# Optimization experiments

Hardware: AMD Instinct MI355X
Metric: run time of the kernel (lower is better)

Reference implementation:

```python
import jax, jax.numpy as jnp
import numpy as np
from jax import lax

B, H_IMG, W_IMG = 512, 812, 40
HID = 128
NUM_CLASSES = 12
LSTM_IN = 32 * ((W_IMG - 5) // 2 + 1)  # 32 channels * 18 = 576


def setup_inputs() -> dict:
    key = jax.random.key(0)
    ks = jax.random.split(key, 20)
    s = 0.05
    inp = {
        "x": jax.random.normal(ks[0], (B, 1, H_IMG, W_IMG), jnp.float32),
        "conv_w": jax.random.normal(ks[1], (32, 1, 20, 5), jnp.float32) * s,
        "conv_b": jax.random.normal(ks[2], (32,), jnp.float32) * s,
        "Wih0": jax.random.normal(ks[3], (4 * HID, LSTM_IN), jnp.float32) * s,
        "Whh0": jax.random.normal(ks[4], (4 * HID, HID), jnp.float32) * s,
        "bih0": jax.random.normal(ks[5], (4 * HID,), jnp.float32) * s,
        "bhh0": jax.random.normal(ks[6], (4 * HID,), jnp.float32) * s,
        "Wih1": jax.random.normal(ks[7], (4 * HID, HID), jnp.float32) * s,
        "Whh1": jax.random.normal(ks[8], (4 * HID, HID), jnp.float32) * s,
        "bih1": jax.random.normal(ks[9], (4 * HID,), jnp.float32) * s,
        "bhh1": jax.random.normal(ks[10], (4 * HID,), jnp.float32) * s,
        "W_att": jax.random.normal(ks[11], (HID, HID), jnp.float32) * s,
        "b_att": jax.random.normal(ks[12], (HID,), jnp.float32) * s,
        "v_att": jax.random.normal(ks[13], (HID,), jnp.float32) * s,
        "W1": jax.random.normal(ks[14], (64, HID), jnp.float32) * s,
        "b1": jax.random.normal(ks[15], (64,), jnp.float32) * s,
        "W2": jax.random.normal(ks[16], (NUM_CLASSES, 64), jnp.float32) * s,
        "b2": jax.random.normal(ks[17], (NUM_CLASSES,), jnp.float32) * s,
    }
    return inp


def _lstm_layer(seq, Wih, Whh, bih, bhh):
    # seq: (T, B, I); PyTorch gate order i, f, g, o
    T, Bn, _ = seq.shape
    Hd = Whh.shape[1]
    x_proj = jnp.einsum('tbi,gi->tbg', seq, Wih) + bih + bhh  # (T,B,4H)

    def step(carry, xg):
        h, c = carry
        g = xg + h @ Whh.T
        i, f, gg, o = jnp.split(g, 4, axis=-1)
        c = jax.nn.sigmoid(f) * c + jax.nn.sigmoid(i) * jnp.tanh(gg)
        h = jax.nn.sigmoid(o) * jnp.tanh(c)
        return (h, c), h

    init = (jnp.zeros((Bn, Hd), seq.dtype), jnp.zeros((Bn, Hd), seq.dtype))
    _, hs = lax.scan(step, init, x_proj)
    return hs  # (T,B,H)


def _forward(x, conv_w, conv_b, Wih0, Whh0, bih0, bhh0, Wih1, Whh1, bih1, bhh1,
             W_att, b_att, v_att, W1, b1, W2, b2):
    # Conv2d(1->32, k=(20,5), s=(8,2)) + ReLU
    y = lax.conv_general_dilated(x, conv_w, (8, 2), 'VALID',
                                 dimension_numbers=('NCHW', 'OIHW', 'NCHW'))
    y = jax.nn.relu(y + conv_b[None, :, None, None])  # (B,32,T,W')
    b, c, t, w = y.shape
    # permute(0,2,3,1).view(b,t,-1).permute(1,0,2) -> (T,B,W'*32)
    seq = jnp.transpose(y, (2, 0, 3, 1)).reshape(t, b, w * c)
    # 2-layer LSTM (inter-layer dropout=0.2 inactive at eval)
    h1 = _lstm_layer(seq, Wih0, Whh0, bih0, bhh0)
    h2 = _lstm_layer(h1, Wih1, Whh1, bih1, bhh1)
    # additive attention pooling over time
    squish = jnp.tanh(jnp.einsum('tbh,hk->tbk', h2, W_att) + b_att)  # (T,B,H)
    attn = jnp.einsum('tbh,h->tb', squish, v_att)                     # (T,B)
    w_att_n = jax.nn.softmax(attn, axis=0)                            # softmax over T
    pooled = jnp.einsum('tb,tbh->bh', w_att_n, h2)                    # (B,H)
    # dnn1 -> (dropout inactive at eval) -> output
    hdn = pooled @ W1.T + b1
    return hdn @ W2.T + b2  # (B,num_classes)


def reference(x, conv_w, conv_b, Wih0, Whh0, bih0, bhh0, Wih1, Whh1, bih1, bhh1,
              W_att, b_att, v_att, W1, b1, W2, b2):
    return _forward(x, conv_w, conv_b, Wih0, Whh0, bih0, bhh0, Wih1, Whh1,
                    bih1, bhh1, W_att, b_att, v_att, W1, b1, W2, b2)
```

## Files before the change

kernel.cpp:

```cpp
#include <hip/hip_runtime.h>
#include <stdint.h>


#define T_STEPS 100
#define BATCH   512
#define HIDD    128
#define GATES   512
#define LSTMIN  576
#define HIMG    812
#define WIMG    40

typedef __attribute__((ext_vector_type(8))) short bf16x8;
typedef __attribute__((ext_vector_type(4))) float f32x4;
typedef __attribute__((ext_vector_type(2))) __fp16 f16x2;
typedef unsigned long long ull;

__device__ inline unsigned short f2bf(float f) {
  unsigned u = __float_as_uint(f);
  unsigned r = (u + 0x7fffu + ((u >> 16) & 1u)) >> 16;
  return (unsigned short)r;
}
__device__ inline unsigned pk_bf16(float a, float b) {
#if __has_builtin(__builtin_amdgcn_cvt_pk_bf16_f32)
  auto r = __builtin_amdgcn_cvt_pk_bf16_f32(a, b);
  return __builtin_bit_cast(unsigned, r);
#else
  return (unsigned)f2bf(a) | ((unsigned)f2bf(b) << 16);
#endif
}
__device__ inline float bf2f(unsigned short b) {
  return __uint_as_float(((unsigned)b) << 16);
}
__device__ inline float fsigm(float x) {
  float e = __expf(-x);
  return __builtin_amdgcn_rcpf(1.f + e);
}
__device__ inline float ftanh(float x) {
  float e = __expf(2.f * x);
  return (e - 1.f) * __builtin_amdgcn_rcpf(e + 1.f);
}
__device__ inline void lds_barrier() {
  asm volatile("s_waitcnt lgkmcnt(0)" ::: "memory");
  __builtin_amdgcn_s_barrier();
}
__device__ inline void wait_flag(int* fp, int need) {
  if ((threadIdx.x & 63) == 0) {
    while (__hip_atomic_load(fp, __ATOMIC_RELAXED, __HIP_MEMORY_SCOPE_AGENT) < need)
      __builtin_amdgcn_s_sleep(2);
  }
  asm volatile("" ::: "memory");
}

__global__ void prep_kernel(const float* __restrict__ Wih0, const float* __restrict__ Whh0,
                            const float* __restrict__ Wih1, const float* __restrict__ Whh1,
                            const float* __restrict__ Watt, const float* __restrict__ convw,
                            const float* __restrict__ bih0, const float* __restrict__ bhh0,
                            const float* __restrict__ bih1, const float* __restrict__ bhh1,
                            unsigned short* __restrict__ wih0b, unsigned short* __restrict__ whh0b,
                            unsigned short* __restrict__ wih1b, unsigned short* __restrict__ whh1b,
                            unsigned short* __restrict__ wattb, f16x2* __restrict__ wpair,
                            float* __restrict__ bias0, float* __restrict__ bias1,
                            int* __restrict__ flags) {
  int tid = blockIdx.x * blockDim.x + threadIdx.x;
  int stride = gridDim.x * blockDim.x;
  for (int i = tid; i < GATES * LSTMIN; i += stride) wih0b[i] = f2bf(Wih0[i]);
  for (int i = tid; i < GATES * HIDD; i += stride) whh0b[i] = f2bf(Whh0[i]);
  for (int i = tid; i < GATES * HIDD; i += stride) wih1b[i] = f2bf(Wih1[i]);
  for (int i = tid; i < GATES * HIDD; i += stride) whh1b[i] = f2bf(Whh1[i]);
  for (int i = tid; i < HIDD * HIDD; i += stride) {
    int j = i >> 7, k = i & 127;
    wattb[i] = f2bf(Watt[k * HIDD + j]);
  }
  for (int i = tid; i < 50 * 32; i += stride) {
    int k2 = i >> 5, c = i & 31;
    int kh2 = k2 / 5, kw = k2 % 5;
    float lo = convw[c * 100 + (2 * kh2) * 5 + kw];
    float hi = convw[c * 100 + (2 * kh2 + 1) * 5 + kw];
    wpair[i] = __builtin_amdgcn_cvt_pkrtz(lo, hi);
  }
  for (int i = tid; i < GATES; i += stride) bias0[i] = bih0[i] + bhh0[i];
  for (int i = tid; i < GATES; i += stride) bias1[i] = bih1[i] + bhh1[i];
  for (int i = tid; i < 32; i += stride) flags[i] = 0;
}

__global__ __launch_bounds__(256) void conv_kernel(const float* __restrict__ x,
                                                   const f16x2* __restrict__ wpair,
                                                   const float* __restrict__ convb,
                                                   unsigned short* __restrict__ seq) {
  __shared__ f16x2 imgp[106 * WIMG];
  const int b = blockIdx.x;
  const int chunk = blockIdx.y;
  const int t0 = chunk * 25;
  const float* src = x + (size_t)b * (HIMG * WIMG) + (size_t)(8 * t0) * WIMG;
  for (int i = threadIdx.x; i < 106 * WIMG; i += 256) {
    int r2 = i / WIMG, c = i % WIMG;
    float lo = src[(2 * r2) * WIMG + c];
    float hi = src[(2 * r2 + 1) * WIMG + c];
    imgp[i] = __builtin_amdgcn_cvt_pkrtz(lo, hi);
  }
  __syncthreads();
  for (int p = threadIdx.x; p < 450; p += 256) {
    int tl = p / 18, wp = p % 18;
    int t = t0 + tl;
    float acc[32];
#pragma unroll
    for (int c = 0; c < 32; ++c) acc[c] = 0.f;
    const f16x2* ibase = imgp + (4 * tl) * WIMG + 2 * wp;
#pragma unroll 2
    for (int kh2 = 0; kh2 < 10; ++kh2) {
#pragma unroll
      for (int kw = 0; kw < 5; ++kw) {
        f16x2 iv = ibase[kh2 * WIMG + kw];
        const f16x2* wk = wpair + (kh2 * 5 + kw) * 32;
#pragma unroll
        for (int c = 0; c < 32; ++c)
          acc[c] = __builtin_amdgcn_fdot2(iv, wk[c], acc[c], false);
      }
    }
    unsigned short* o = seq + ((size_t)(t * BATCH + b)) * LSTMIN + wp * 32;
#pragma unroll
    for (int c = 0; c < 32; ++c) {
      float v = acc[c] + convb[c];
      o[c] = f2bf(v > 0.f ? v : 0.f);
    }
  }
}

template <int KDIM>
__global__ __launch_bounds__(256) void gemm_xp_kernel(const unsigned short* __restrict__ A,
                                                      const unsigned short* __restrict__ Bw,
                                                      const float* __restrict__ bias,
                                                      unsigned short* __restrict__ Xp) {
  __shared__ __align__(16) unsigned short As[128 * 32];
  __shared__ __align__(16) unsigned short Bs[128 * 32];
  const int tid = threadIdx.x;
  const int lane = tid & 63;
  const int w = tid >> 6;
  const int col16 = lane & 15;
  const int q = lane >> 4;
  const int n0 = blockIdx.x * 128;
  const int m0 = blockIdx.y * 128;
  const int wm = (w & 1) * 64;
  const int wn = (w >> 1) * 64;
  f32x4 acc[4][4] = {};
  const int r = tid >> 2;
  const int sw = ((tid & 3) ^ (r & 3)) * 8;
  const unsigned wslot = (unsigned)w * 512;
  const unsigned short* ga = A + (size_t)(m0 + r) * KDIM + sw;
  const unsigned short* gb = Bw + (size_t)(n0 + r) * KDIM + sw;
  for (int k0 = 0; k0 < KDIM; k0 += 32) {
    __syncthreads();
    __builtin_amdgcn_global_load_lds((const __attribute__((address_space(1))) void*)(ga + k0),
                                     (__attribute__((address_space(3))) void*)(As + wslot), 16, 0, 0);
    __builtin_amdgcn_global_load_lds((const __attribute__((address_space(1))) void*)(ga + k0 + (size_t)64 * KDIM),
                                     (__attribute__((address_space(3))) void*)(As + wslot + 2048), 16, 0, 0);
    __builtin_amdgcn_global_load_lds((const __attribute__((address_space(1))) void*)(gb + k0),
                                     (__attribute__((address_space(3))) void*)(Bs + wslot), 16, 0, 0);
    __builtin_amdgcn_global_load_lds((const __attribute__((address_space(1))) void*)(gb + k0 + (size_t)64 * KDIM),
                                     (__attribute__((address_space(3))) void*)(Bs + wslot + 2048), 16, 0, 0);
    __syncthreads();
    bf16x8 af[4], bv[4];
#pragma unroll
    for (int i = 0; i < 4; ++i) {
      int ra = wm + i * 16 + col16;
      af[i] = *(const bf16x8*)(As + ra * 32 + ((q ^ (ra & 3)) * 8));
      int rb2 = wn + i * 16 + col16;
      bv[i] = *(const bf16x8*)(Bs + rb2 * 32 + ((q ^ (rb2 & 3)) * 8));
    }
#pragma unroll
    for (int i = 0; i < 4; ++i)
#pragma unroll
      for (int j = 0; j < 4; ++j)
        acc[i][j] = __builtin_amdgcn_mfma_f32_16x16x32_bf16(af[i], bv[j], acc[i][j], 0, 0, 0);
  }
#pragma unroll
  for (int ct = 0; ct < 4; ++ct) {
    int n = n0 + wn + ct * 16 + col16;
    float bvv = bias[n];
    int wS = (n >> 4) & 7;
    int ntS = n >> 7;
    int c16S = n & 15;
#pragma unroll
    for (int rt = 0; rt < 4; ++rt) {
      int m = m0 + wm + rt * 16 + q * 4;
      int t = m >> 9;
      int bb = m & 511;
      int blk = bb >> 4;
      int r16 = bb & 15;
      ushort4 u;
      u.x = f2bf(acc[rt][ct][0] + bvv);
      u.y = f2bf(acc[rt][ct][1] + bvv);
      u.z = f2bf(acc[rt][ct][2] + bvv);
      u.w = f2bf(acc[rt][ct][3] + bvv);
      size_t tile = (((size_t)t * 32 + blk) * 8 + wS) * 4 + ntS;
      *(ushort4*)(Xp + tile * 256 + c16S * 16 + r16) = u;
    }
  }
}

__global__ __launch_bounds__(512, 1) void scan_pipe_kernel(
    const unsigned short* __restrict__ Xp0, const unsigned short* __restrict__ Whh0,
    const unsigned short* __restrict__ Wih1, const float* __restrict__ bias1,
    unsigned short* __restrict__ Xp1, const unsigned short* __restrict__ Whh1,
    unsigned short* __restrict__ hout, int* __restrict__ flags) {
  __shared__ __align__(16) unsigned short hb[2][16 * 136];
  const int tid = threadIdx.x;
  const int lane = tid & 63;
  const int w = tid >> 6;
  const int col16 = lane & 15;
  const int q = lane >> 4;
  const bool producer = blockIdx.x < 32;
  const int blk = producer ? (int)blockIdx.x : (int)blockIdx.x - 32;
  const int rb = blk * 16;
  const int hc = w * 16 + col16;
  const int srow = tid >> 5;
  const int scol = (tid & 31) * 4;
  int* flagp = flags + blk;

  if (producer) {
    bf16x8 bfrag[4][4], bfrag2[4][4];
    const unsigned short* xpb[4];
    ull* xob[4];
    float biasn[4];
#pragma unroll
    for (int nt = 0; nt < 4; ++nt) {
      int cn = nt * HIDD + hc;
#pragma unroll
      for (int ks = 0; ks < 4; ++ks) {
        bfrag[nt][ks] = *(const bf16x8*)(Whh0 + (size_t)cn * HIDD + ks * 32 + q * 8);
        bfrag2[nt][ks] = *(const bf16x8*)(Wih1 + (size_t)cn * HIDD + ks * 32 + q * 8);
      }
      biasn[nt] = bias1[cn];
      size_t tile = (((size_t)blk) * 8 + w) * 4 + nt;
      xpb[nt] = Xp0 + tile * 256 + col16 * 16 + q * 4;
      xob[nt] = (ull*)(Xp1 + tile * 256 + col16 * 16 + q * 4);
    }
    uint2 xb[2][4];
#pragma unroll
    for (int nt = 0; nt < 4; ++nt) xb[0][nt] = *(const uint2*)(xpb[nt]);
#pragma unroll
    for (int nt = 0; nt < 4; ++nt) xb[1][nt] = *(const uint2*)(xpb[nt] + GATES * BATCH);
    for (int i = tid; i < 2 * 16 * 136; i += 512) hb[0][i] = 0;
    float cst[4] = {0.f, 0.f, 0.f, 0.f};
    ull pend[4] = {0, 0, 0, 0};
    lds_barrier();

#pragma unroll 4
    for (int t = 0; t < T_STEPS; ++t) {
      if (t >= 2) {
#pragma unroll
        for (int nt = 0; nt < 4; ++nt)
          __hip_atomic_store(xob[nt] + (size_t)(t - 2) * (GATES * BATCH / 4), pend[nt],
                             __ATOMIC_RELAXED, __HIP_MEMORY_SCOPE_AGENT);
      }
      asm volatile("" ::: "memory");
      const int s = t & 1;
      uint2 xv[4];
#pragma unroll
      for (int nt = 0; nt < 4; ++nt) xv[nt] = xb[s][nt];
      if (t + 2 < T_STEPS) {
#pragma unroll
        for (int nt = 0; nt < 4; ++nt)
          xb[s][nt] = *(const uint2*)(xpb[nt] + (size_t)(t + 2) * (GATES * BATCH));
      }
      asm volatile("" ::: "memory");
      const int pb = (t & 1) ^ 1;
      bf16x8 af[4];
#pragma unroll
      for (int ks = 0; ks < 4; ++ks)
        af[ks] = *(const bf16x8*)(hb[pb] + col16 * 136 + ks * 32 + q * 8);
      f32x4 acc[4];
#pragma unroll
      for (int nt = 0; nt < 4; ++nt) {
        acc[nt][0] = __uint_as_float(xv[nt].x << 16);
        acc[nt][1] = __uint_as_float(xv[nt].x & 0xffff0000u);
        acc[nt][2] = __uint_as_float(xv[nt].y << 16);
        acc[nt][3] = __uint_as_float(xv[nt].y & 0xffff0000u);
      }
#pragma unroll
      for (int ks = 0; ks < 4; ++ks)
#pragma unroll
        for (int nt = 0; nt < 4; ++nt)
          acc[nt] = __builtin_amdgcn_mfma_f32_16x16x32_bf16(af[ks], bfrag[nt][ks], acc[nt], 0, 0, 0);
      f32x4 acc2[4];
#pragma unroll
      for (int nt = 0; nt < 4; ++nt) acc2[nt] = f32x4{0.f, 0.f, 0.f, 0.f};
#pragma unroll
      for (int ks = 0; ks < 4; ++ks)
#pragma unroll
        for (int nt = 0; nt < 4; ++nt)
          acc2[nt] = __builtin_amdgcn_mfma_f32_16x16x32_bf16(af[ks], bfrag2[nt][ks], acc2[nt], 0, 0, 0);
      unsigned short hv[4];
#pragma unroll
      for (int rr = 0; rr < 4; ++rr) {
        float pi = acc[0][rr], pf = acc[1][rr];
        float pg = acc[2][rr], po = acc[3][rr];
        float cc = fsigm(pf) * cst[rr] + fsigm(pi) * ftanh(pg);
        cst[rr] = cc;
        hv[rr] = f2bf(fsigm(po) * ftanh(cc));
      }
#pragma unroll
      for (int nt = 0; nt < 4; ++nt) {
        unsigned lo = pk_bf16(acc2[nt][0] + biasn[nt], acc2[nt][1] + biasn[nt]);
        unsigned hi = pk_bf16(acc2[nt][2] + biasn[nt], acc2[nt][3] + biasn[nt]);
        pend[nt] = (ull)lo | ((ull)hi << 32);
      }
#pragma unroll
      for (int rr = 0; rr < 4; ++rr)
        hb[t & 1][(q * 4 + rr) * 136 + hc] = hv[rr];
      if ((t & 3) == 3 && t < 99) {
        asm volatile("s_waitcnt vmcnt(4) lgkmcnt(0)\ns_barrier" ::: "memory");
        if (tid == 0)
          __hip_atomic_store(flagp, t, __ATOMIC_RELAXED, __HIP_MEMORY_SCOPE_AGENT);
      } else {
        lds_barrier();
      }
    }
#pragma unroll
    for (int nt = 0; nt < 4; ++nt)
      __hip_atomic_store(xob[nt] + (size_t)98 * (GATES * BATCH / 4), pend[nt],
                         __ATOMIC_RELAXED, __HIP_MEMORY_SCOPE_AGENT);
    bf16x8 af[4];
#pragma unroll
    for (int ks = 0; ks < 4; ++ks)
      af[ks] = *(const bf16x8*)(hb[(T_STEPS - 1) & 1] + col16 * 136 + ks * 32 + q * 8);
    f32x4 acc2[4];
#pragma unroll
    for (int nt = 0; nt < 4; ++nt) acc2[nt] = f32x4{0.f, 0.f, 0.f, 0.f};
#pragma unroll
    for (int ks = 0; ks < 4; ++ks)
#pragma unroll
      for (int nt = 0; nt < 4; ++nt)
        acc2[nt] = __builtin_amdgcn_mfma_f32_16x16x32_bf16(af[ks], bfrag2[nt][ks], acc2[nt], 0, 0, 0);
#pragma unroll
    for (int nt = 0; nt < 4; ++nt) {
      unsigned lo = pk_bf16(acc2[nt][0] + biasn[nt], acc2[nt][1] + biasn[nt]);
      unsigned hi = pk_bf16(acc2[nt][2] + biasn[nt], acc2[nt][3] + biasn[nt]);
      __hip_atomic_store(xob[nt] + (size_t)99 * (GATES * BATCH / 4),
                         (ull)lo | ((ull)hi << 32),
                         __ATOMIC_RELAXED, __HIP_MEMORY_SCOPE_AGENT);
    }
    asm volatile("s_waitcnt vmcnt(0) lgkmcnt(0)\ns_barrier" ::: "memory");
    if (tid == 0)
      __hip_atomic_store(flagp, 101, __ATOMIC_RELAXED, __HIP_MEMORY_SCOPE_AGENT);
  } else {
    bf16x8 bfrag[4][4];
    ull* xpb[4];
#pragma unroll
    for (int nt = 0; nt < 4; ++nt) {
      int cn = nt * HIDD + hc;
#pragma unroll
      for (int ks = 0; ks < 4; ++ks)
        bfrag[nt][ks] = *(const bf16x8*)(Whh1 + (size_t)cn * HIDD + ks * 32 + q * 8);
      size_t tile = (((size_t)blk) * 8 + w) * 4 + nt;
      xpb[nt] = (ull*)(Xp1 + tile * 256 + col16 * 16 + q * 4);
    }
    for (int i = tid; i < 2 * 16 * 136; i += 512) hb[0][i] = 0;
    wait_flag(flagp, 7);
    ull xb[2][4];
#pragma unroll
    for (int nt = 0; nt < 4; ++nt)
      xb[0][nt] = __hip_atomic_load(xpb[nt], __ATOMIC_RELAXED, __HIP_MEMORY_SCOPE_AGENT);
#pragma unroll
    for (int nt = 0; nt < 4; ++nt)
      xb[1][nt] = __hip_atomic_load(xpb[nt] + (GATES * BATCH / 4), __ATOMIC_RELAXED, __HIP_MEMORY_SCOPE_AGENT);
    float cst[4] = {0.f, 0.f, 0.f, 0.f};
    lds_barrier();

#pragma unroll 4
    for (int t = 0; t < T_STEPS; ++t) {
      if (t > 0 && (t & 3) == 0) {
        int need = t + 7;
        if (need > 101) need = 101;
        wait_flag(flagp, need);
      }
      const int pb = (t & 1) ^ 1;
      bf16x8 af[4];
#pragma unroll
      for (int ks = 0; ks < 4; ++ks)
        af[ks] = *(const bf16x8*)(hb[pb] + col16 * 136 + ks * 32 + q * 8);
      if (t > 0) {
        ushort4 hx = *(const ushort4*)(hb[pb] + srow * 136 + scol);
        *(ushort4*)(hout + ((size_t)((t - 1) * BATCH) + rb + srow) * HIDD + scol) = hx;
      }
      const int s = t & 1;
      ull xv[4];
#pragma unroll
      for (int nt = 0; nt < 4; ++nt) xv[nt] = xb[s][nt];
      if (t + 2 < T_STEPS) {
#pragma unroll
        for (int nt = 0; nt < 4; ++nt)
          xb[s][nt] = __hip_atomic_load(xpb[nt] + (size_t)(t + 2) * (GATES * BATCH / 4),
                                        __ATOMIC_RELAXED, __HIP_MEMORY_SCOPE_AGENT);
      }
      f32x4 acc[4];
#pragma unroll
      for (int nt = 0; nt < 4; ++nt) {
        unsigned lo = (unsigned)xv[nt];
        unsigned hi = (unsigned)(xv[nt] >> 32);
        acc[nt][0] = __uint_as_float(lo << 16);
        acc[nt][1] = __uint_as_float(lo & 0xffff0000u);
        acc[nt][2] = __uint_as_float(hi << 16);
        acc[nt][3] = __uint_as_float(hi & 0xffff0000u);
      }
#pragma unroll
      for (int ks = 0; ks < 4; ++ks)
#pragma unroll
        for (int nt = 0; nt < 4; ++nt)
          acc[nt] = __builtin_amdgcn_mfma_f32_16x16x32_bf16(af[ks], bfrag[nt][ks], acc[nt], 0, 0, 0);
      unsigned short hv[4];
#pragma unroll
      for (int rr = 0; rr < 4; ++rr) {
        float pi = acc[0][rr], pf = acc[1][rr];
        float pg = acc[2][rr], po = acc[3][rr];
        float cc = fsigm(pf) * cst[rr] + fsigm(pi) * ftanh(pg);
        cst[rr] = cc;
        hv[rr] = f2bf(fsigm(po) * ftanh(cc));
      }
#pragma unroll
      for (int rr = 0; rr < 4; ++rr)
        hb[t & 1][(q * 4 + rr) * 136 + hc] = hv[rr];
      lds_barrier();
    }
    ushort4 hx = *(const ushort4*)(hb[(T_STEPS - 1) & 1] + srow * 136 + scol);
    *(ushort4*)(hout + ((size_t)((T_STEPS - 1) * BATCH) + rb + srow) * HIDD + scol) = hx;
  }
}

__global__ __launch_bounds__(256) void gemm_att_kernel(const unsigned short* __restrict__ A,
                                                       const unsigned short* __restrict__ Bw,
                                                       const float* __restrict__ b_att,
                                                       const float* __restrict__ v_att,
                                                       float* __restrict__ scores) {
  __shared__ __align__(16) unsigned short As[128 * 32];
  __shared__ __align__(16) unsigned short Bs[128 * 32];
  __shared__ float s_red[128];
  const int tid = threadIdx.x;
  const int lane = tid & 63;
  const int w = tid >> 6;
  const int col16 = lane & 15;
  const int q = lane >> 4;
  const int m0 = blockIdx.y * 128;
  const int wm = (w & 1) * 64;
  const int wn = (w >> 1) * 64;
  f32x4 acc[4][4] = {};
  const int r = tid >> 2;
  const int sw = ((tid & 3) ^ (r & 3)) * 8;
  const unsigned wslot = (unsigned)w * 512;
  const unsigned short* ga = A + (size_t)(m0 + r) * HIDD + sw;
  const unsigned short* gb = Bw + (size_t)r * HIDD + sw;
  for (int k0 = 0; k0 < HIDD; k0 += 32) {
    __syncthreads();
    __builtin_amdgcn_global_load_lds((const __attribute__((address_space(1))) void*)(ga + k0),
                                     (__attribute__((address_space(3))) void*)(As + wslot), 16, 0, 0);
    __builtin_amdgcn_global_load_lds((const __attribute__((address_space(1))) void*)(ga + k0 + (size_t)64 * HIDD),
                                     (__attribute__((address_space(3))) void*)(As + wslot + 2048), 16, 0, 0);
    __builtin_amdgcn_global_load_lds((const __attribute__((address_space(1))) void*)(gb + k0),
                                     (__attribute__((address_space(3))) void*)(Bs + wslot), 16, 0, 0);
    __builtin_amdgcn_global_load_lds((const __attribute__((address_space(1))) void*)(gb + k0 + (size_t)64 * HIDD),
                                     (__attribute__((address_space(3))) void*)(Bs + wslot + 2048), 16, 0, 0);
    __syncthreads();
    bf16x8 af[4], bv[4];
#pragma unroll
    for (int i = 0; i < 4; ++i) {
      int ra = wm + i * 16 + col16;
      af[i] = *(const bf16x8*)(As + ra * 32 + ((q ^ (ra & 3)) * 8));
      int rb2 = wn + i * 16 + col16;
      bv[i] = *(const bf16x8*)(Bs + rb2 * 32 + ((q ^ (rb2 & 3)) * 8));
    }
#pragma unroll
    for (int i = 0; i < 4; ++i)
#pragma unroll
      for (int j = 0; j < 4; ++j)
        acc[i][j] = __builtin_amdgcn_mfma_f32_16x16x32_bf16(af[i], bv[j], acc[i][j], 0, 0, 0);
  }
  if (tid < 128) s_red[tid] = 0.f;
  float rs[4][4];
#pragma unroll
  for (int rt = 0; rt < 4; ++rt)
#pragma unroll
    for (int rr = 0; rr < 4; ++rr) rs[rt][rr] = 0.f;
#pragma unroll
  for (int ct = 0; ct < 4; ++ct) {
    int n = wn + ct * 16 + col16;
    float bvv = b_att[n], vv = v_att[n];
#pragma unroll
    for (int rt = 0; rt < 4; ++rt)
#pragma unroll
      for (int rr = 0; rr < 4; ++rr) {
        float xv2 = acc[rt][ct][rr] + bvv;
        float e = __expf(2.f * xv2);
        rs[rt][rr] += vv * (e - 1.f) * __builtin_amdgcn_rcpf(e + 1.f);
      }
  }
#pragma unroll
  for (int off = 1; off < 16; off <<= 1)
#pragma unroll
    for (int rt = 0; rt < 4; ++rt)
#pragma unroll
      for (int rr = 0; rr < 4; ++rr) rs[rt][rr] += __shfl_xor(rs[rt][rr], off, 64);
  __syncthreads();
  if (col16 == 0) {
#pragma unroll
    for (int rt = 0; rt < 4; ++rt)
#pragma unroll
      for (int rr = 0; rr < 4; ++rr)
        atomicAdd(&s_red[wm + rt * 16 + q * 4 + rr], rs[rt][rr]);
  }
  __syncthreads();
  if (tid < 128) scores[m0 + tid] = s_red[tid];
}

__global__ __launch_bounds__(128) void final_kernel(const float* __restrict__ scores,
                                                    const unsigned short* __restrict__ h2,
                                                    const float* __restrict__ W1, const float* __restrict__ b1,
                                                    const float* __restrict__ W2, const float* __restrict__ b2,
                                                    float* __restrict__ out) {
  const int b = blockIdx.x;
  const int tid = threadIdx.x;
  __shared__ float wj[T_STEPS];
  __shared__ float red[128];
  __shared__ float pooled[128];
  __shared__ float hdn[64];
  float sv = (tid < T_STEPS) ? scores[tid * BATCH + b] : -1e30f;
  red[tid] = sv;
  __syncthreads();
#pragma unroll
  for (int off = 64; off > 0; off >>= 1) {
    if (tid < off) red[tid] = fmaxf(red[tid], red[tid + off]);
    __syncthreads();
  }
  float mx = red[0];
  __syncthreads();
  float ev = (tid < T_STEPS) ? __expf(sv - mx) : 0.f;
  red[tid] = ev;
  __syncthreads();
#pragma unroll
  for (int off = 64; off > 0; off >>= 1) {
    if (tid < off) red[tid] += red[tid + off];
    __syncthreads();
  }
  float inv = 1.0f / red[0];
  if (tid < T_STEPS) wj[tid] = ev * inv;
  __syncthreads();
  float p = 0.f;
  for (int t = 0; t < T_STEPS; ++t)
    p += wj[t] * bf2f(h2[((size_t)(t * BATCH + b)) * HIDD + tid]);
  pooled[tid] = p;
  __syncthreads();
  if (tid < 64) {
    float a = b1[tid];
    for (int h = 0; h < 128; ++h) a = fmaf(W1[tid * 128 + h], pooled[h], a);
    hdn[tid] = a;
  }
  __syncthreads();
  if (tid < 12) {
    float a = b2[tid];
    for (int j = 0; j < 64; ++j) a = fmaf(W2[tid * 64 + j], hdn[j], a);
    out[b * 12 + tid] = a;
  }
}

extern "C" void kernel_launch(void* const* d_in, const int* in_sizes, int n_in,
                              void* d_out, int out_size, void* d_ws, size_t ws_size,
                              hipStream_t stream) {
  (void)in_sizes; (void)n_in; (void)out_size; (void)ws_size;
  const float* x      = (const float*)d_in[0];
  const float* conv_w = (const float*)d_in[1];
  const float* conv_b = (const float*)d_in[2];
  const float* Wih0   = (const float*)d_in[3];
  const float* Whh0   = (const float*)d_in[4];
  const float* bih0   = (const float*)d_in[5];
  const float* bhh0   = (const float*)d_in[6];
  const float* Wih1   = (const float*)d_in[7];
  const float* Whh1   = (const float*)d_in[8];
  const float* bih1   = (const float*)d_in[9];
  const float* bhh1   = (const float*)d_in[10];
  const float* W_att  = (const float*)d_in[11];
  const float* b_att  = (const float*)d_in[12];
  const float* v_att  = (const float*)d_in[13];
  const float* W1     = (const float*)d_in[14];
  const float* b1     = (const float*)d_in[15];
  const float* W2     = (const float*)d_in[16];
  const float* b2     = (const float*)d_in[17];

  char* ws = (char*)d_ws;
  size_t off = 0;
  auto carve = [&](size_t bytes) { char* p = ws + off; off += (bytes + 255) & ~(size_t)255; return p; };
  unsigned short* seq    = (unsigned short*)carve((size_t)T_STEPS * BATCH * LSTMIN * 2);
  unsigned short* xp0    = (unsigned short*)carve((size_t)T_STEPS * GATES * BATCH * 2);
  unsigned short* h2     = (unsigned short*)carve((size_t)T_STEPS * BATCH * HIDD * 2);
  float*          scores = (float*)carve((size_t)T_STEPS * BATCH * 4);
  unsigned short* wih0b  = (unsigned short*)carve((size_t)GATES * LSTMIN * 2);
  unsigned short* whh0b  = (unsigned short*)carve((size_t)GATES * HIDD * 2);
  unsigned short* wih1b  = (unsigned short*)carve((size_t)GATES * HIDD * 2);
  unsigned short* whh1b  = (unsigned short*)carve((size_t)GATES * HIDD * 2);
  unsigned short* wattb  = (unsigned short*)carve((size_t)HIDD * HIDD * 2);
  f16x2*          wpair  = (f16x2*)carve(50 * 32 * 4);
  float*          bias0  = (float*)carve(GATES * 4);
  float*          bias1  = (float*)carve(GATES * 4);
  int*            flags  = (int*)carve(32 * 4);
  unsigned short* xp1 = seq;

  prep_kernel<<<256, 256, 0, stream>>>(Wih0, Whh0, Wih1, Whh1, W_att, conv_w,
                                       bih0, bhh0, bih1, bhh1,
                                       wih0b, whh0b, wih1b, whh1b, wattb, wpair,
                                       bias0, bias1, flags);
  conv_kernel<<<dim3(512, 4), 256, 0, stream>>>(x, wpair, conv_b, seq);
  gemm_xp_kernel<LSTMIN><<<dim3(4, 400), 256, 0, stream>>>(seq, wih0b, bias0, xp0);
  scan_pipe_kernel<<<64, 512, 0, stream>>>(xp0, whh0b, wih1b, bias1, xp1, whh1b, h2, flags);
  gemm_att_kernel<<<dim3(1, 400), 256, 0, stream>>>(h2, wattb, b_att, v_att, scores);
  final_kernel<<<512, 128, 0, stream>>>(scores, h2, W1, b1, W2, b2, (float*)d_out);
}
```

Before: 412.6 us.

## Split scan block warps into recurrence and side-task roles with 32-column ownership

The pipelined LSTM scan kernel now gives warps two roles. In the layer-0 block, four warps run the Whh0 recurrence, each owning 32 hidden columns across all four gates, while the other four warps compute the Wih1 projection one step behind and publish it. In the layer-1 block, four warps run the recurrence and four only copy h out to global memory. The Xp tile layout in the input GEMM is reordered to match the new per-warp ownership, launch bounds allow two blocks per CU, and the flag thresholds change. This takes the projection and store work off the recurrence critical path, at the cost of doubling per-warp MFMA and register load on the recurrence warps.

```diff
diff --git a/kernel.cpp b/kernel.cpp
--- a/kernel.cpp
+++ b/kernel.cpp
@@ -177,28 +177,30 @@
   for (int ct = 0; ct < 4; ++ct) {
     int n = n0 + wn + ct * 16 + col16;
     float bvv = bias[n];
-    int wS = (n >> 4) & 7;
-    int ntS = n >> 7;
+    int g = n >> 7;
+    int rr2 = n & 127;
+    int wqS = rr2 >> 5;
+    int ntS = g * 2 + ((rr2 >> 4) & 1);
     int c16S = n & 15;
 #pragma unroll
     for (int rt = 0; rt < 4; ++rt) {
       int m = m0 + wm + rt * 16 + q * 4;
       int t = m >> 9;
       int bb = m & 511;
-      int blk = bb >> 4;
+      int blkS = bb >> 4;
       int r16 = bb & 15;
       ushort4 u;
       u.x = f2bf(acc[rt][ct][0] + bvv);
       u.y = f2bf(acc[rt][ct][1] + bvv);
       u.z = f2bf(acc[rt][ct][2] + bvv);
       u.w = f2bf(acc[rt][ct][3] + bvv);
-      size_t tile = (((size_t)t * 32 + blk) * 8 + wS) * 4 + ntS;
+      size_t tile = (((size_t)t * 32 + blkS) * 4 + wqS) * 8 + ntS;
       *(ushort4*)(Xp + tile * 256 + c16S * 16 + r16) = u;
     }
   }
 }
 
-__global__ __launch_bounds__(512, 1) void scan_pipe_kernel(
+__global__ __launch_bounds__(512, 2) void scan_pipe_kernel(
     const unsigned short* __restrict__ Xp0, const unsigned short* __restrict__ Whh0,
     const unsigned short* __restrict__ Wih1, const float* __restrict__ bias1,
     unsigned short* __restrict__ Xp1, const unsigned short* __restrict__ Whh1,
@@ -207,223 +209,250 @@
   const int tid = threadIdx.x;
   const int lane = tid & 63;
   const int w = tid >> 6;
+  const int wq = w & 3;
+  const int role = w >> 2;
   const int col16 = lane & 15;
   const int q = lane >> 4;
   const bool producer = blockIdx.x < 32;
   const int blk = producer ? (int)blockIdx.x : (int)blockIdx.x - 32;
   const int rb = blk * 16;
-  const int hc = w * 16 + col16;
-  const int srow = tid >> 5;
-  const int scol = (tid & 31) * 4;
   int* flagp = flags + blk;
+  const size_t TSTRIDE = (size_t)GATES * BATCH;
+  const size_t TSTRIDE8 = TSTRIDE / 4;
+
+  {
+    unsigned short* hz = (unsigned short*)hb;
+    for (int i = tid; i < 2 * 16 * 136; i += 512) hz[i] = 0;
+  }
 
   if (producer) {
-    bf16x8 bfrag[4][4], bfrag2[4][4];
-    const unsigned short* xpb[4];
-    ull* xob[4];
-    float biasn[4];
-#pragma unroll
-    for (int nt = 0; nt < 4; ++nt) {
-      int cn = nt * HIDD + hc;
-#pragma unroll
-      for (int ks = 0; ks < 4; ++ks) {
-        bfrag[nt][ks] = *(const bf16x8*)(Whh0 + (size_t)cn * HIDD + ks * 32 + q * 8);
-        bfrag2[nt][ks] = *(const bf16x8*)(Wih1 + (size_t)cn * HIDD + ks * 32 + q * 8);
-      }
-      biasn[nt] = bias1[cn];
-      size_t tile = (((size_t)blk) * 8 + w) * 4 + nt;
-      xpb[nt] = Xp0 + tile * 256 + col16 * 16 + q * 4;
-      xob[nt] = (ull*)(Xp1 + tile * 256 + col16 * 16 + q * 4);
+    if (role == 0) {
+      bf16x8 bfrag[8][4];
+      const unsigned short* xpb[8];
+#pragma unroll
+      for (int nt = 0; nt < 8; ++nt) {
+        int cn = (nt >> 1) * HIDD + wq * 32 + (nt & 1) * 16 + col16;
+#pragma unroll
+        for (int ks = 0; ks < 4; ++ks)
+          bfrag[nt][ks] = *(const bf16x8*)(Whh0 + (size_t)cn * HIDD + ks * 32 + q * 8);
+        size_t tile = (((size_t)blk) * 4 + wq) * 8 + nt;
+        xpb[nt] = Xp0 + tile * 256 + col16 * 16 + q * 4;
+      }
+      uint2 xb[2][8];
+#pragma unroll
+      for (int nt = 0; nt < 8; ++nt) xb[0][nt] = *(const uint2*)(xpb[nt]);
+#pragma unroll
+      for (int nt = 0; nt < 8; ++nt) xb[1][nt] = *(const uint2*)(xpb[nt] + TSTRIDE);
+      float cst[8] = {0.f, 0.f, 0.f, 0.f, 0.f, 0.f, 0.f, 0.f};
+      lds_barrier();
+#pragma unroll 2
+      for (int t = 0; t < T_STEPS; ++t) {
+        const int s = t & 1;
+        uint2 xv[8];
+#pragma unroll
+        for (int nt = 0; nt < 8; ++nt) xv[nt] = xb[s][nt];
+        if (t + 2 < T_STEPS) {
+#pragma unroll
+          for (int nt = 0; nt < 8; ++nt)
+            xb[s][nt] = *(const uint2*)(xpb[nt] + (size_t)(t + 2) * TSTRIDE);
+        }
+        bf16x8 af[4];
+#pragma unroll
+        for (int ks = 0; ks < 4; ++ks)
+          af[ks] = *(const bf16x8*)(hb[s ^ 1] + col16 * 136 + ks * 32 + q * 8);
+        f32x4 acc[8];
+#pragma unroll
+        for (int nt = 0; nt < 8; ++nt) {
+          acc[nt][0] = __uint_as_float(xv[nt].x << 16);
+          acc[nt][1] = __uint_as_float(xv[nt].x & 0xffff0000u);
+          acc[nt][2] = __uint_as_float(xv[nt].y << 16);
+          acc[nt][3] = __uint_as_float(xv[nt].y & 0xffff0000u);
+        }
+#pragma unroll
+        for (int ks = 0; ks < 4; ++ks)
+#pragma unroll
+          for (int nt = 0; nt < 8; ++nt)
+            acc[nt] = __builtin_amdgcn_mfma_f32_16x16x32_bf16(af[ks], bfrag[nt][ks], acc[nt], 0, 0, 0);
+#pragma unroll
+        for (int hh = 0; hh < 2; ++hh)
+#pragma unroll
+          for (int rr = 0; rr < 4; ++rr) {
+            int idx = hh * 4 + rr;
+            float pi = acc[0 + hh][rr];
+            float pf = acc[2 + hh][rr];
+            float pg = acc[4 + hh][rr];
+            float po = acc[6 + hh][rr];
+            float cc = fsigm(pf) * cst[idx] + fsigm(pi) * ftanh(pg);
+            cst[idx] = cc;
+            hb[s][(q * 4 + rr) * 136 + wq * 32 + hh * 16 + col16] = f2bf(fsigm(po) * ftanh(cc));
+          }
+        lds_barrier();
+      }
+      lds_barrier();
+    } else {
+      bf16x8 bfrag2[8][4];
+      float biasn[8];
+      ull* xob[8];
+#pragma unroll
+      for (int nt = 0; nt < 8; ++nt) {
+        int cn = (nt >> 1) * HIDD + wq * 32 + (nt & 1) * 16 + col16;
+#pragma unroll
+        for (int ks = 0; ks < 4; ++ks)
+          bfrag2[nt][ks] = *(const bf16x8*)(Wih1 + (size_t)cn * HIDD + ks * 32 + q * 8);
+        biasn[nt] = bias1[cn];
+        size_t tile = (((size_t)blk) * 4 + wq) * 8 + nt;
+        xob[nt] = (ull*)(Xp1 + tile * 256 + col16 * 16 + q * 4);
+      }
+      lds_barrier();
+#pragma unroll 2
+      for (int t = 0; t < T_STEPS; ++t) {
+        const int s = t & 1;
+        if (t > 0) {
+          bf16x8 af[4];
+#pragma unroll
+          for (int ks = 0; ks < 4; ++ks)
+            af[ks] = *(const bf16x8*)(hb[s ^ 1] + col16 * 136 + ks * 32 + q * 8);
+          f32x4 acc2[8];
+#pragma unroll
+          for (int nt = 0; nt < 8; ++nt) acc2[nt] = f32x4{0.f, 0.f, 0.f, 0.f};
+#pragma unroll
+          for (int ks = 0; ks < 4; ++ks)
+#pragma unroll
+            for (int nt = 0; nt < 8; ++nt)
+              acc2[nt] = __builtin_amdgcn_mfma_f32_16x16x32_bf16(af[ks], bfrag2[nt][ks], acc2[nt], 0, 0, 0);
+#pragma unroll
+          for (int nt = 0; nt < 8; ++nt) {
+            unsigned lo = pk_bf16(acc2[nt][0] + biasn[nt], acc2[nt][1] + biasn[nt]);
+            unsigned hi = pk_bf16(acc2[nt][2] + biasn[nt], acc2[nt][3] + biasn[nt]);
+            __hip_atomic_store(xob[nt] + (size_t)(t - 1) * TSTRIDE8,
+                               (ull)lo | ((ull)hi << 32),
+                               __ATOMIC_RELAXED, __HIP_MEMORY_SCOPE_AGENT);
+          }
+        }
+        if ((t & 3) == 3) {
+          asm volatile("s_waitcnt vmcnt(0) lgkmcnt(0)\ns_barrier" ::: "memory");
+          if (tid == 256)
+            __hip_atomic_store(flagp, t, __ATOMIC_RELAXED, __HIP_MEMORY_SCOPE_AGENT);
+        } else {
+          lds_barrier();
+        }
+      }
+      {
+        bf16x8 af[4];
+#pragma unroll
+        for (int ks = 0; ks < 4; ++ks)
+          af[ks] = *(const bf16x8*)(hb[(T_STEPS - 1) & 1] + col16 * 136 + ks * 32 + q * 8);
+        f32x4 acc2[8];
+#pragma unroll
+        for (int nt = 0; nt < 8; ++nt) acc2[nt] = f32x4{0.f, 0.f, 0.f, 0.f};
+#pragma unroll
+        for (int ks = 0; ks < 4; ++ks)
+#pragma unroll
+          for (int nt = 0; nt < 8; ++nt)
+            acc2[nt] = __builtin_amdgcn_mfma_f32_16x16x32_bf16(af[ks], bfrag2[nt][ks], acc2[nt], 0, 0, 0);
+#pragma unroll
+        for (int nt = 0; nt < 8; ++nt) {
+          unsigned lo = pk_bf16(acc2[nt][0] + biasn[nt], acc2[nt][1] + biasn[nt]);
+          unsigned hi = pk_bf16(acc2[nt][2] + biasn[nt], acc2[nt][3] + biasn[nt]);
+          __hip_atomic_store(xob[nt] + (size_t)(T_STEPS - 1) * TSTRIDE8,
+                             (ull)lo | ((ull)hi << 32),
+                             __ATOMIC_RELAXED, __HIP_MEMORY_SCOPE_AGENT);
+        }
+        asm volatile("s_waitcnt vmcnt(0) lgkmcnt(0)\ns_barrier" ::: "memory");
+        if (tid == 256)
+          __hip_atomic_store(flagp, 100, __ATOMIC_RELAXED, __HIP_MEMORY_SCOPE_AGENT);
+      }
     }
-    uint2 xb[2][4];
-#pragma unroll
-    for (int nt = 0; nt < 4; ++nt) xb[0][nt] = *(const uint2*)(xpb[nt]);
-#pragma unroll
-    for (int nt = 0; nt < 4; ++nt) xb[1][nt] = *(const uint2*)(xpb[nt] + GATES * BATCH);
-    for (int i = tid; i < 2 * 16 * 136; i += 512) hb[0][i] = 0;
-    float cst[4] = {0.f, 0.f, 0.f, 0.f};
-    ull pend[4] = {0, 0, 0, 0};
-    lds_barrier();
-
-#pragma unroll 4
-    for (int t = 0; t < T_STEPS; ++t) {
-      if (t >= 2) {
-#pragma unroll
-        for (int nt = 0; nt < 4; ++nt)
-          __hip_atomic_store(xob[nt] + (size_t)(t - 2) * (GATES * BATCH / 4), pend[nt],
-                             __ATOMIC_RELAXED, __HIP_MEMORY_SCOPE_AGENT);
-      }
-      asm volatile("" ::: "memory");
-      const int s = t & 1;
-      uint2 xv[4];
-#pragma unroll
-      for (int nt = 0; nt < 4; ++nt) xv[nt] = xb[s][nt];
-      if (t + 2 < T_STEPS) {
-#pragma unroll
-        for (int nt = 0; nt < 4; ++nt)
-          xb[s][nt] = *(const uint2*)(xpb[nt] + (size_t)(t + 2) * (GATES * BATCH));
-      }
-      asm volatile("" ::: "memory");
-      const int pb = (t & 1) ^ 1;
-      bf16x8 af[4];
-#pragma unroll
-      for (int ks = 0; ks < 4; ++ks)
-        af[ks] = *(const bf16x8*)(hb[pb] + col16 * 136 + ks * 32 + q * 8);
-      f32x4 acc[4];
-#pragma unroll
-      for (int nt = 0; nt < 4; ++nt) {
-        acc[nt][0] = __uint_as_float(xv[nt].x << 16);
-        acc[nt][1] = __uint_as_float(xv[nt].x & 0xffff0000u);
-        acc[nt][2] = __uint_as_float(xv[nt].y << 16);
-        acc[nt][3] = __uint_as_float(xv[nt].y & 0xffff0000u);
-      }
-#pragma unroll
-      for (int ks = 0; ks < 4; ++ks)
-#pragma unroll
-        for (int nt = 0; nt < 4; ++nt)
-          acc[nt] = __builtin_amdgcn_mfma_f32_16x16x32_bf16(af[ks], bfrag[nt][ks], acc[nt], 0, 0, 0);
-      f32x4 acc2[4];
-#pragma unroll
-      for (int nt = 0; nt < 4; ++nt) acc2[nt] = f32x4{0.f, 0.f, 0.f, 0.f};
-#pragma unroll
-      for (int ks = 0; ks < 4; ++ks)
-#pragma unroll
-        for (int nt = 0; nt < 4; ++nt)
-          acc2[nt] = __builtin_amdgcn_mfma_f32_16x16x32_bf16(af[ks], bfrag2[nt][ks], acc2[nt], 0, 0, 0);
-      unsigned short hv[4];
-#pragma unroll
-      for (int rr = 0; rr < 4; ++rr) {
-        float pi = acc[0][rr], pf = acc[1][rr];
-        float pg = acc[2][rr], po = acc[3][rr];
-        float cc = fsigm(pf) * cst[rr] + fsigm(pi) * ftanh(pg);
-        cst[rr] = cc;
-        hv[rr] = f2bf(fsigm(po) * ftanh(cc));
-      }
-#pragma unroll
-      for (int nt = 0; nt < 4; ++nt) {
-        unsigned lo = pk_bf16(acc2[nt][0] + biasn[nt], acc2[nt][1] + biasn[nt]);
-        unsigned hi = pk_bf16(acc2[nt][2] + biasn[nt], acc2[nt][3] + biasn[nt]);
-        pend[nt] = (ull)lo | ((ull)hi << 32);
-      }
-#pragma unroll
-      for (int rr = 0; rr < 4; ++rr)
-        hb[t & 1][(q * 4 + rr) * 136 + hc] = hv[rr];
-      if ((t & 3) == 3 && t < 99) {
-        asm volatile("s_waitcnt vmcnt(4) lgkmcnt(0)\ns_barrier" ::: "memory");
-        if (tid == 0)
-          __hip_atomic_store(flagp, t, __ATOMIC_RELAXED, __HIP_MEMORY_SCOPE_AGENT);
-      } else {
+  } else {
+    if (role == 0) {
+      bf16x8 bfrag[8][4];
+      ull* xpb[8];
+#pragma unroll
+      for (int nt = 0; nt < 8; ++nt) {
+        int cn = (nt >> 1) * HIDD + wq * 32 + (nt & 1) * 16 + col16;
+#pragma unroll
+        for (int ks = 0; ks < 4; ++ks)
+          bfrag[nt][ks] = *(const bf16x8*)(Whh1 + (size_t)cn * HIDD + ks * 32 + q * 8);
+        size_t tile = (((size_t)blk) * 4 + wq) * 8 + nt;
+        xpb[nt] = (ull*)(Xp1 + tile * 256 + col16 * 16 + q * 4);
+      }
+      wait_flag(flagp, 6);
+      ull xb[2][8];
+#pragma unroll
+      for (int nt = 0; nt < 8; ++nt)
+        xb[0][nt] = __hip_atomic_load(xpb[nt], __ATOMIC_RELAXED, __HIP_MEMORY_SCOPE_AGENT);
+#pragma unroll
+      for (int nt = 0; nt < 8; ++nt)
+        xb[1][nt] = __hip_atomic_load(xpb[nt] + TSTRIDE8, __ATOMIC_RELAXED, __HIP_MEMORY_SCOPE_AGENT);
+      float cst[8] = {0.f, 0.f, 0.f, 0.f, 0.f, 0.f, 0.f, 0.f};
+      lds_barrier();
+#pragma unroll 2
+      for (int t = 0; t < T_STEPS; ++t) {
+        if (t > 0 && (t & 3) == 0) {
+          int need = t + 6;
+          if (need > 100) need = 100;
+          wait_flag(flagp, need);
+        }
+        const int s = t & 1;
+        ull xv[8];
+#pragma unroll
+        for (int nt = 0; nt < 8; ++nt) xv[nt] = xb[s][nt];
+        if (t + 2 < T_STEPS) {
+#pragma unroll
+          for (int nt = 0; nt < 8; ++nt)
+            xb[s][nt] = __hip_atomic_load(xpb[nt] + (size_t)(t + 2) * TSTRIDE8,
+                                          __ATOMIC_RELAXED, __HIP_MEMORY_SCOPE_AGENT);
+        }
+        bf16x8 af[4];
+#pragma unroll
+        for (int ks = 0; ks < 4; ++ks)
+          af[ks] = *(const bf16x8*)(hb[s ^ 1] + col16 * 136 + ks * 32 + q * 8);
+        f32x4 acc[8];
+#pragma unroll
+        for (int nt = 0; nt < 8; ++nt) {
+          unsigned lo = (unsigned)xv[nt];
+          unsigned hi = (unsigned)(xv[nt] >> 32);
+          acc[nt][0] = __uint_as_float(lo << 16);
+          acc[nt][1] = __uint_as_float(lo & 0xffff0000u);
+          acc[nt][2] = __uint_as_float(hi << 16);
+          acc[nt][3] = __uint_as_float(hi & 0xffff0000u);
+        }
+#pragma unroll
+        for (int ks = 0; ks < 4; ++ks)
+#pragma unroll
+          for (int nt = 0; nt < 8; ++nt)
+            acc[nt] = __builtin_amdgcn_mfma_f32_16x16x32_bf16(af[ks], bfrag[nt][ks], acc[nt], 0, 0, 0);
+#pragma unroll
+        for (int hh = 0; hh < 2; ++hh)
+#pragma unroll
+          for (int rr = 0; rr < 4; ++rr) {
+            int idx = hh * 4 + rr;
+            float pi = acc[0 + hh][rr];
+            float pf = acc[2 + hh][rr];
+            float pg = acc[4 + hh][rr];
+            float po = acc[6 + hh][rr];
+            float cc = fsigm(pf) * cst[idx] + fsigm(pi) * ftanh(pg);
+            cst[idx] = cc;
+            hb[s][(q * 4 + rr) * 136 + wq * 32 + hh * 16 + col16] = f2bf(fsigm(po) * ftanh(cc));
+          }
         lds_barrier();
       }
+    } else {
+      const int c = wq * 64 + lane;
+      const int row = c >> 4;
+      const int ch = c & 15;
+      lds_barrier();
+#pragma unroll 2
+      for (int t = 0; t < T_STEPS; ++t) {
+        if (t > 0) {
+          uint4 hx = *(const uint4*)(hb[(t - 1) & 1] + row * 136 + ch * 8);
+          *(uint4*)(hout + ((size_t)((t - 1) * BATCH) + rb + row) * HIDD + ch * 8) = hx;
+        }
+        lds_barrier();
+      }
+      uint4 hx = *(const uint4*)(hb[(T_STEPS - 1) & 1] + row * 136 + ch * 8);
+      *(uint4*)(hout + ((size_t)((T_STEPS - 1) * BATCH) + rb + row) * HIDD + ch * 8) = hx;
     }
-#pragma unroll
-    for (int nt = 0; nt < 4; ++nt)
-      __hip_atomic_store(xob[nt] + (size_t)98 * (GATES * BATCH / 4), pend[nt],
-                         __ATOMIC_RELAXED, __HIP_MEMORY_SCOPE_AGENT);
-    bf16x8 af[4];
-#pragma unroll
-    for (int ks = 0; ks < 4; ++ks)
-      af[ks] = *(const bf16x8*)(hb[(T_STEPS - 1) & 1] + col16 * 136 + ks * 32 + q * 8);
-    f32x4 acc2[4];
-#pragma unroll
-    for (int nt = 0; nt < 4; ++nt) acc2[nt] = f32x4{0.f, 0.f, 0.f, 0.f};
-#pragma unroll
-    for (int ks = 0; ks < 4; ++ks)
-#pragma unroll
-      for (int nt = 0; nt < 4; ++nt)
-        acc2[nt] = __builtin_amdgcn_mfma_f32_16x16x32_bf16(af[ks], bfrag2[nt][ks], acc2[nt], 0, 0, 0);
-#pragma unroll
-    for (int nt = 0; nt < 4; ++nt) {
-      unsigned lo = pk_bf16(acc2[nt][0] + biasn[nt], acc2[nt][1] + biasn[nt]);
-      unsigned hi = pk_bf16(acc2[nt][2] + biasn[nt], acc2[nt][3] + biasn[nt]);
-      __hip_atomic_store(xob[nt] + (size_t)99 * (GATES * BATCH / 4),
-                         (ull)lo | ((ull)hi << 32),
-                         __ATOMIC_RELAXED, __HIP_MEMORY_SCOPE_AGENT);
-    }
-    asm volatile("s_waitcnt vmcnt(0) lgkmcnt(0)\ns_barrier" ::: "memory");
-    if (tid == 0)
-      __hip_atomic_store(flagp, 101, __ATOMIC_RELAXED, __HIP_MEMORY_SCOPE_AGENT);
-  } else {
-    bf16x8 bfrag[4][4];
-    ull* xpb[4];
-#pragma unroll
-    for (int nt = 0; nt < 4; ++nt) {
-      int cn = nt * HIDD + hc;
-#pragma unroll
-      for (int ks = 0; ks < 4; ++ks)
-        bfrag[nt][ks] = *(const bf16x8*)(Whh1 + (size_t)cn * HIDD + ks * 32 + q * 8);
-      size_t tile = (((size_t)blk) * 8 + w) * 4 + nt;
-      xpb[nt] = (ull*)(Xp1 + tile * 256 + col16 * 16 + q * 4);
-    }
-    for (int i = tid; i < 2 * 16 * 136; i += 512) hb[0][i] = 0;
-    wait_flag(flagp, 7);
-    ull xb[2][4];
-#pragma unroll
-    for (int nt = 0; nt < 4; ++nt)
-      xb[0][nt] = __hip_atomic_load(xpb[nt], __ATOMIC_RELAXED, __HIP_MEMORY_SCOPE_AGENT);
-#pragma unroll
-    for (int nt = 0; nt < 4; ++nt)
-      xb[1][nt] = __hip_atomic_load(xpb[nt] + (GATES * BATCH / 4), __ATOMIC_RELAXED, __HIP_MEMORY_SCOPE_AGENT);
-    float cst[4] = {0.f, 0.f, 0.f, 0.f};
-    lds_barrier();
-
-#pragma unroll 4
-    for (int t = 0; t < T_STEPS; ++t) {
-      if (t > 0 && (t & 3) == 0) {
-        int need = t + 7;
-        if (need > 101) need = 101;
-        wait_flag(flagp, need);
-      }
-      const int pb = (t & 1) ^ 1;
-      bf16x8 af[4];
-#pragma unroll
-      for (int ks = 0; ks < 4; ++ks)
-        af[ks] = *(const bf16x8*)(hb[pb] + col16 * 136 + ks * 32 + q * 8);
-      if (t > 0) {
-        ushort4 hx = *(const ushort4*)(hb[pb] + srow * 136 + scol);
-        *(ushort4*)(hout + ((size_t)((t - 1) * BATCH) + rb + srow) * HIDD + scol) = hx;
-      }
-      const int s = t & 1;
-      ull xv[4];
-#pragma unroll
-      for (int nt = 0; nt < 4; ++nt) xv[nt] = xb[s][nt];
-      if (t + 2 < T_STEPS) {
-#pragma unroll
-        for (int nt = 0; nt < 4; ++nt)
-          xb[s][nt] = __hip_atomic_load(xpb[nt] + (size_t)(t + 2) * (GATES * BATCH / 4),
-                                        __ATOMIC_RELAXED, __HIP_MEMORY_SCOPE_AGENT);
-      }
-      f32x4 acc[4];
-#pragma unroll
-      for (int nt = 0; nt < 4; ++nt) {
-        unsigned lo = (unsigned)xv[nt];
-        unsigned hi = (unsigned)(xv[nt] >> 32);
-        acc[nt][0] = __uint_as_float(lo << 16);
-        acc[nt][1] = __uint_as_float(lo & 0xffff0000u);
-        acc[nt][2] = __uint_as_float(hi << 16);
-        acc[nt][3] = __uint_as_float(hi & 0xffff0000u);
-      }
-#pragma unroll
-      for (int ks = 0; ks < 4; ++ks)
-#pragma unroll
-        for (int nt = 0; nt < 4; ++nt)
-          acc[nt] = __builtin_amdgcn_mfma_f32_16x16x32_bf16(af[ks], bfrag[nt][ks], acc[nt], 0, 0, 0);
-      unsigned short hv[4];
-#pragma unroll
-      for (int rr = 0; rr < 4; ++rr) {
-        float pi = acc[0][rr], pf = acc[1][rr];
-        float pg = acc[2][rr], po = acc[3][rr];
-        float cc = fsigm(pf) * cst[rr] + fsigm(pi) * ftanh(pg);
-        cst[rr] = cc;
-        hv[rr] = f2bf(fsigm(po) * ftanh(cc));
-      }
-#pragma unroll
-      for (int rr = 0; rr < 4; ++rr)
-        hb[t & 1][(q * 4 + rr) * 136 + hc] = hv[rr];
-      lds_barrier();
-    }
-    ushort4 hx = *(const ushort4*)(hb[(T_STEPS - 1) & 1] + srow * 136 + scol);
-    *(ushort4*)(hout + ((size_t)((T_STEPS - 1) * BATCH) + rb + srow) * HIDD + scol) = hx;
   }
 }
 
@@ -544,6 +573,7 @@
   if (tid < T_STEPS) wj[tid] = ev * inv;
   __syncthreads();
   float p = 0.f;
+#pragma unroll 4
   for (int t = 0; t < T_STEPS; ++t)
     p += wj[t] * bf2f(h2[((size_t)(t * BATCH + b)) * HIDD + tid]);
   pooled[tid] = p;
```

Result: slower. 421.1 us (+2.0%).
